# Performance work log

Measured on AMD Instinct MI355X. Metric: run time of the kernel, lower is better.

## Reference

```python
import jax, jax.numpy as jnp
import numpy as np


def _unfold3(x):
    # x: (B, 1, H, W) -> (B, 9, L), L=(H-2)*(W-2); kernel positions row-major (matches torch Unfold)
    B, _, H, W = x.shape
    patches = jnp.stack(
        [x[:, 0, i:H - 2 + i, j:W - 2 + j] for i in range(3) for j in range(3)], axis=1
    )  # (B, 9, H-2, W-2)
    return patches.reshape(B, 9, (H - 2) * (W - 2))


def setup_inputs() -> dict:
    key = jax.random.key(0)
    k1, k2, k3 = jax.random.split(key, 3)
    B, H, Wd = 16, 64, 64
    D = 32  # dendrite
    x = jax.random.uniform(k1, (B, 1, H, Wd), dtype=jnp.float32) * 255.0
    W = 0.01 * jnp.abs(jax.random.normal(k2, (D, 18, 4), dtype=jnp.float32)) + 0.2
    q = 0.01 * jnp.abs(jax.random.normal(k3, (D, 18, 4), dtype=jnp.float32)) + 0.0
    return {"x": x, "W": W, "q": q}


def reference(x, W, q):
    K_SYN = 10.0   # DConvSynaps k
    K_SOMA = 10.0  # DConvSoma slope
    p = _unfold3(x)                   # (B, 9, L)
    center = p[:, 4:5, :]             # (B, 1, L) center pixel of each 3x3 patch
    # torch.isclose(p, center, rtol=0, atol=3) -> |p - center| <= 3
    x1 = (jnp.abs(p - center) <= 3.0).astype(p.dtype)
    x1 = x1.at[:, 4, :].set(1.0)
    feat = jnp.concatenate([x1, p], axis=1)            # (B, 18, L)
    # DConvSynaps broadcast: (B, L, 1, 18, 1) against W,q (D, 18, 4)
    xb = feat.transpose(0, 2, 1)[:, :, None, :, None]  # (B, L, 1, 18, 1)
    syn = jax.nn.sigmoid((xb * W - q) * K_SYN)         # (B, L, D, 18, 4)
    dend = jnp.prod(syn, axis=3)                       # (B, L, D, 4)
    menb = jnp.sum(dend, axis=2)                       # (B, L, 4)
    soma = jax.nn.sigmoid((menb - 0.5) * K_SOMA)       # (B, L, 4)
    return jnp.sum(soma, axis=1)                       # (B, 4)
```

## Files before the change

kernel.cpp:

```cpp
#include <hip/hip_runtime.h>
#include <math.h>

#define LOG2E 1.44269504088896340736f

__global__ __launch_bounds__(256, 4)
void orientation_kernel(const float* __restrict__ x,
                        const float* __restrict__ Wm,
                        const float* __restrict__ qm,
                        float* __restrict__ out)
{
    const int blk  = blockIdx.x;
    const int b    = blk / 62;
    const int r    = blk - b * 62;
    const int tid  = threadIdx.x;
    const int wave = tid >> 6;
    const int lane = tid & 63;
    const int d    = lane & 31;
    const int kh   = lane >> 5;

    __shared__ float xs[3][64];
    __shared__ float red[4][4];

    if (tid < 192) {
        const int row = tid >> 6;
        const int col = tid & 63;
        xs[row][col] = x[b * 4096 + (r + row) * 64 + col];
    }
    __syncthreads();

    float s0v[2][9], dsv[2][9], Wc[2][9], qc[2][9];
#pragma unroll
    for (int kk = 0; kk < 2; ++kk) {
        const int k = kh + 2 * kk;
        const int base = d * 72;
#pragma unroll
        for (int j = 0; j < 9; ++j) {
            const float w0 = Wm[base + j * 4 + k];
            const float q0 = qm[base + j * 4 + k];
            const float e0 = __builtin_amdgcn_exp2f( 10.f * LOG2E * q0);
            const float s0 = __builtin_amdgcn_rcpf(1.f + e0);
            const float e1 = __builtin_amdgcn_exp2f(-10.f * LOG2E * (w0 - q0));
            const float s1 = __builtin_amdgcn_rcpf(1.f + e1);
            s0v[kk][j] = s0;
            dsv[kk][j] = s1 - s0;
            const float w1 = Wm[base + (9 + j) * 4 + k];
            const float q1 = qm[base + (9 + j) * 4 + k];
            Wc[kk][j] = -10.f * LOG2E * w1;
            qc[kk][j] =  10.f * LOG2E * q1;
        }
    }

    float acc0 = 0.f, acc1 = 0.f;

    const int c0 = wave * 16;
    const int c1 = (c0 + 16 < 62) ? (c0 + 16) : 62;

    for (int c = c0; c < c1; ++c) {
        float p[9];
#pragma unroll
        for (int i = 0; i < 3; ++i)
#pragma unroll
            for (int jj = 0; jj < 3; ++jj)
                p[i * 3 + jj] = xs[i][c + jj];
        const float ctr = p[4];

        float prodB0 = 1.f, prodB1 = 1.f;
        float prodA0 = 1.f, prodA1 = 1.f;
#pragma unroll
        for (int j = 0; j < 9; ++j) {
            const float x1f = (fabsf(p[j] - ctr) <= 3.0f) ? 1.f : 0.f;
            prodB0 *= fmaf(x1f, dsv[0][j], s0v[0][j]);
            prodB1 *= fmaf(x1f, dsv[1][j], s0v[1][j]);
            const float eA0 = __builtin_amdgcn_exp2f(fmaf(p[j], Wc[0][j], qc[0][j]));
            const float eA1 = __builtin_amdgcn_exp2f(fmaf(p[j], Wc[1][j], qc[1][j]));
            prodA0 = fmaf(prodA0, eA0, prodA0);
            prodA1 = fmaf(prodA1, eA1, prodA1);
        }
        float dend0 = prodB0 * __builtin_amdgcn_rcpf(prodA0);
        float dend1 = prodB1 * __builtin_amdgcn_rcpf(prodA1);

#pragma unroll
        for (int m = 1; m <= 16; m <<= 1) {
            dend0 += __shfl_xor(dend0, m, 64);
            dend1 += __shfl_xor(dend1, m, 64);
        }

        const float soma0 = __builtin_amdgcn_rcpf(
            1.f + __builtin_amdgcn_exp2f((0.5f - dend0) * (10.f * LOG2E)));
        const float soma1 = __builtin_amdgcn_rcpf(
            1.f + __builtin_amdgcn_exp2f((0.5f - dend1) * (10.f * LOG2E)));
        acc0 += soma0;
        acc1 += soma1;
    }

    if ((lane & 31) == 0) {
        red[wave][kh]     = acc0;
        red[wave][kh + 2] = acc1;
    }
    __syncthreads();

    if (tid < 4) {
        const float s = red[0][tid] + red[1][tid] + red[2][tid] + red[3][tid];
        atomicAdd(&out[b * 4 + tid], s);
    }
}

extern "C" void kernel_launch(void* const* d_in, const int* in_sizes, int n_in,
                              void* d_out, int out_size, void* d_ws, size_t ws_size,
                              hipStream_t stream) {
    const float* x  = (const float*)d_in[0];
    const float* Wm = (const float*)d_in[1];
    const float* qm = (const float*)d_in[2];
    float* out = (float*)d_out;

    const int B = in_sizes[0] / (64 * 64);

    hipMemsetAsync(d_out, 0, (size_t)out_size * sizeof(float), stream);

    dim3 grid(B * 62);
    dim3 block(256);
    orientation_kernel<<<grid, block, 0, stream>>>(x, Wm, qm, out);
}
```

Baseline: 52.65 us.

## Remap threads to pixel-per-lane with dendrite loop and shared param table

Switches the work decomposition from lanes over dendrites (with a shuffle reduction over 32 dendrites per pixel) to lanes over pixels, with each wave handling one output channel k and looping over all 32 dendrites serially. The per-(k,d,j) sigmoid constants are precomputed once per block into a 4608-entry float4 shared-memory table, and the center tap is special-cased. This removes the per-pixel cross-lane reductions and their soma work per chunk. In exchange, every block recomputes the full parameter table, which costs 4608 exp/rcp pairs plus global reads before any pixel work starts, and the inner loop now issues many LDS float4 loads.

```diff
diff --git a/kernel.cpp b/kernel.cpp
--- a/kernel.cpp
+++ b/kernel.cpp
@@ -2,6 +2,13 @@
 #include <math.h>
 
 #define LOG2E 1.44269504088896340736f
+
+constexpr int IMG  = 64;
+constexpr int OW   = 62;
+constexpr int NPIX = 62 * 62;
+constexpr int D    = 32;
+constexpr int K    = 4;
+constexpr int CHUNKS = (NPIX + 63) / 64;
 
 __global__ __launch_bounds__(256, 4)
 void orientation_kernel(const float* __restrict__ x,
@@ -9,100 +16,86 @@
                         const float* __restrict__ qm,
                         float* __restrict__ out)
 {
-    const int blk  = blockIdx.x;
-    const int b    = blk / 62;
-    const int r    = blk - b * 62;
-    const int tid  = threadIdx.x;
-    const int wave = tid >> 6;
-    const int lane = tid & 63;
-    const int d    = lane & 31;
-    const int kh   = lane >> 5;
+    __shared__ float4 tbl[K * D * 9];
 
-    __shared__ float xs[3][64];
-    __shared__ float red[4][4];
+    const int tid = threadIdx.x;
 
-    if (tid < 192) {
-        const int row = tid >> 6;
-        const int col = tid & 63;
-        xs[row][col] = x[b * 4096 + (r + row) * 64 + col];
+    for (int t = tid; t < K * D * 9; t += 256) {
+        const int j = t % 9;
+        const int dk = t / 9;
+        const int d = dk % D;
+        const int k = dk / D;
+        const int base = d * 72;
+
+        const float w0 = Wm[base + j * 4 + k];
+        const float q0 = qm[base + j * 4 + k];
+        const float s1 = __builtin_amdgcn_rcpf(
+            1.f + __builtin_amdgcn_exp2f(-10.f * LOG2E * (w0 - q0)));
+        float s0, ds;
+        if (j == 4) {
+            s0 = s1; ds = 0.f;
+        } else {
+            s0 = __builtin_amdgcn_rcpf(
+                1.f + __builtin_amdgcn_exp2f(10.f * LOG2E * q0));
+            ds = s1 - s0;
+        }
+        const float w1 = Wm[base + (9 + j) * 4 + k];
+        const float q1 = qm[base + (9 + j) * 4 + k];
+        tbl[t] = make_float4(s0, ds, -10.f * LOG2E * w1, 10.f * LOG2E * q1);
     }
     __syncthreads();
 
-    float s0v[2][9], dsv[2][9], Wc[2][9], qc[2][9];
+    const int lane = tid & 63;
+    const int k    = tid >> 6;
+    const int b     = blockIdx.x / CHUNKS;
+    const int chunk = blockIdx.x - b * CHUNKS;
+
+    const int pi    = chunk * 64 + lane;
+    const bool valid = (pi < NPIX);
+    const int pic   = valid ? pi : (NPIX - 1);
+    const int row   = pic / OW;
+    const int col   = pic - row * OW;
+
+    const float* xb = x + b * IMG * IMG;
+    float p[9];
 #pragma unroll
-    for (int kk = 0; kk < 2; ++kk) {
-        const int k = kh + 2 * kk;
-        const int base = d * 72;
+    for (int i = 0; i < 3; ++i)
+#pragma unroll
+        for (int jj = 0; jj < 3; ++jj)
+            p[i * 3 + jj] = xb[(row + i) * IMG + col + jj];
+
+    const float ctr = p[4];
+    float x1f[9];
+#pragma unroll
+    for (int j = 0; j < 9; ++j)
+        x1f[j] = (fabsf(p[j] - ctr) <= 3.0f) ? 1.f : 0.f;
+
+    const float4* tk = &tbl[k * D * 9];
+    float menb = 0.f;
+#pragma unroll 2
+    for (int d = 0; d < D; ++d) {
+        float prodB = 1.f;
+        float prodA = 1.f;
 #pragma unroll
         for (int j = 0; j < 9; ++j) {
-            const float w0 = Wm[base + j * 4 + k];
-            const float q0 = qm[base + j * 4 + k];
-            const float e0 = __builtin_amdgcn_exp2f( 10.f * LOG2E * q0);
-            const float s0 = __builtin_amdgcn_rcpf(1.f + e0);
-            const float e1 = __builtin_amdgcn_exp2f(-10.f * LOG2E * (w0 - q0));
-            const float s1 = __builtin_amdgcn_rcpf(1.f + e1);
-            s0v[kk][j] = s0;
-            dsv[kk][j] = s1 - s0;
-            const float w1 = Wm[base + (9 + j) * 4 + k];
-            const float q1 = qm[base + (9 + j) * 4 + k];
-            Wc[kk][j] = -10.f * LOG2E * w1;
-            qc[kk][j] =  10.f * LOG2E * q1;
+            const float4 c = tk[d * 9 + j];
+            prodB *= fmaf(x1f[j], c.y, c.x);
+            const float e = __builtin_amdgcn_exp2f(fmaf(p[j], c.z, c.w));
+            prodA = fmaf(prodA, e, prodA);
         }
+        menb += prodB * __builtin_amdgcn_rcpf(prodA);
     }
 
-    float acc0 = 0.f, acc1 = 0.f;
-
-    const int c0 = wave * 16;
-    const int c1 = (c0 + 16 < 62) ? (c0 + 16) : 62;
-
-    for (int c = c0; c < c1; ++c) {
-        float p[9];
-#pragma unroll
-        for (int i = 0; i < 3; ++i)
-#pragma unroll
-            for (int jj = 0; jj < 3; ++jj)
-                p[i * 3 + jj] = xs[i][c + jj];
-        const float ctr = p[4];
-
-        float prodB0 = 1.f, prodB1 = 1.f;
-        float prodA0 = 1.f, prodA1 = 1.f;
-#pragma unroll
-        for (int j = 0; j < 9; ++j) {
-            const float x1f = (fabsf(p[j] - ctr) <= 3.0f) ? 1.f : 0.f;
-            prodB0 *= fmaf(x1f, dsv[0][j], s0v[0][j]);
-            prodB1 *= fmaf(x1f, dsv[1][j], s0v[1][j]);
-            const float eA0 = __builtin_amdgcn_exp2f(fmaf(p[j], Wc[0][j], qc[0][j]));
-            const float eA1 = __builtin_amdgcn_exp2f(fmaf(p[j], Wc[1][j], qc[1][j]));
-            prodA0 = fmaf(prodA0, eA0, prodA0);
-            prodA1 = fmaf(prodA1, eA1, prodA1);
-        }
-        float dend0 = prodB0 * __builtin_amdgcn_rcpf(prodA0);
-        float dend1 = prodB1 * __builtin_amdgcn_rcpf(prodA1);
+    float soma = __builtin_amdgcn_rcpf(
+        1.f + __builtin_amdgcn_exp2f((0.5f - menb) * (10.f * LOG2E)));
+    if (!valid) soma = 0.f;
 
 #pragma unroll
-        for (int m = 1; m <= 16; m <<= 1) {
-            dend0 += __shfl_xor(dend0, m, 64);
-            dend1 += __shfl_xor(dend1, m, 64);
-        }
+    for (int m = 1; m <= 32; m <<= 1)
+        soma += __shfl_xor(soma, m, 64);
 
-        const float soma0 = __builtin_amdgcn_rcpf(
-            1.f + __builtin_amdgcn_exp2f((0.5f - dend0) * (10.f * LOG2E)));
-        const float soma1 = __builtin_amdgcn_rcpf(
-            1.f + __builtin_amdgcn_exp2f((0.5f - dend1) * (10.f * LOG2E)));
-        acc0 += soma0;
-        acc1 += soma1;
-    }
-
-    if ((lane & 31) == 0) {
-        red[wave][kh]     = acc0;
-        red[wave][kh + 2] = acc1;
-    }
-    __syncthreads();
-
-    if (tid < 4) {
-        const float s = red[0][tid] + red[1][tid] + red[2][tid] + red[3][tid];
-        atomicAdd(&out[b * 4 + tid], s);
-    }
+    if (lane == 0)
+        atomicAdd(&out[b * 4 + k], soma);
 }
 
 extern "C" void kernel_launch(void* const* d_in, const int* in_sizes, int n_in,
@@ -113,11 +106,11 @@
     const float* qm = (const float*)d_in[2];
     float* out = (float*)d_out;
 
-    const int B = in_sizes[0] / (64 * 64);
+    const int B = in_sizes[0] / (IMG * IMG);
 
     hipMemsetAsync(d_out, 0, (size_t)out_size * sizeof(float), stream);
 
-    dim3 grid(B * 62);
+    dim3 grid(B * CHUNKS);
     dim3 block(256);
     orientation_kernel<<<grid, block, 0, stream>>>(x, Wm, qm, out);
 }
```

New measurement: 45.35 us. 1.16x faster.

## Precompute synapse table in prologue kernel, use log-domain binary product and DPP reductions

Applied to the files above, without the earlier changes.

A small prologue kernel now precomputes per-(k,d) constants into workspace: the binary-feature sigmoid factors are turned into log2 terms, so their product becomes a sum of FMAs followed by one exp2. The same kernel zeroes the output, which replaces the memset. The main kernel loads this table with float4 reads instead of recomputing sigmoids in every block. The cross-lane reduction uses DPP adds for the first four steps, work is rebalanced across waves (16/16/15/15 pixels), and each wave issues atomics directly instead of doing a shared-memory block reduction. The tradeoffs are an extra kernel launch, more atomics and higher register use from the 64-entry tables.

```diff
diff --git a/kernel.cpp b/kernel.cpp
--- a/kernel.cpp
+++ b/kernel.cpp
@@ -3,105 +3,142 @@
 
 #define LOG2E 1.44269504088896340736f
 
+constexpr int IMG = 64;
+constexpr int OW  = 62;
+constexpr int D   = 32;
+constexpr int K   = 4;
+
+__global__ void build_table(const float* __restrict__ Wm,
+                            const float* __restrict__ qm,
+                            float* __restrict__ tb,
+                            float* __restrict__ out, int out_n)
+{
+    const int t = threadIdx.x;
+    for (int i = t; i < out_n; i += 128) out[i] = 0.f;
+    if (t >= K * D) return;
+    const int d = t & 31;
+    const int k = t >> 5;
+    const int base = d * 72;
+    float* e = tb + t * 32;
+
+    float cB = 0.f;
+    int jj = 0;
+#pragma unroll
+    for (int j = 0; j < 9; ++j) {
+        const float w0 = Wm[base + j * 4 + k];
+        const float q0 = qm[base + j * 4 + k];
+        const float l1 = -log2f(1.f + __builtin_amdgcn_exp2f(-10.f * LOG2E * (w0 - q0)));
+        if (j == 4) {
+            cB += l1;
+        } else {
+            const float l0 = -log2f(1.f + __builtin_amdgcn_exp2f(10.f * LOG2E * q0));
+            cB += l0;
+            e[jj++] = l1 - l0;
+        }
+        const float w1 = Wm[base + (9 + j) * 4 + k];
+        const float q1 = qm[base + (9 + j) * 4 + k];
+        e[9 + j]  = -10.f * LOG2E * w1;
+        e[18 + j] =  10.f * LOG2E * q1;
+    }
+    e[8] = cB;
+    e[27] = e[28] = e[29] = e[30] = e[31] = 0.f;
+}
+
+template <int CTRL>
+__device__ __forceinline__ float dpp_xadd(float v) {
+    const int t = __builtin_amdgcn_update_dpp(0, __float_as_int(v), CTRL, 0xf, 0xf, true);
+    return v + __int_as_float(t);
+}
+
 __global__ __launch_bounds__(256, 4)
-void orientation_kernel(const float* __restrict__ x,
-                        const float* __restrict__ Wm,
-                        const float* __restrict__ qm,
-                        float* __restrict__ out)
+void orientation_main(const float* __restrict__ x,
+                      const float4* __restrict__ tb,
+                      float* __restrict__ out)
 {
-    const int blk  = blockIdx.x;
-    const int b    = blk / 62;
-    const int r    = blk - b * 62;
     const int tid  = threadIdx.x;
     const int wave = tid >> 6;
     const int lane = tid & 63;
     const int d    = lane & 31;
     const int kh   = lane >> 5;
+    const int b    = blockIdx.x / OW;
+    const int r    = blockIdx.x - b * OW;
 
-    __shared__ float xs[3][64];
-    __shared__ float red[4][4];
-
+    __shared__ float xs[3][IMG];
     if (tid < 192) {
         const int row = tid >> 6;
         const int col = tid & 63;
-        xs[row][col] = x[b * 4096 + (r + row) * 64 + col];
+        xs[row][col] = x[b * IMG * IMG + (r + row) * IMG + col];
+    }
+
+    float E0[32], E1[32];
+    {
+        const float4* t0 = tb + (kh * D + d) * 8;
+        const float4* t1 = t0 + 2 * D * 8;
+#pragma unroll
+        for (int i = 0; i < 8; ++i) {
+            *reinterpret_cast<float4*>(&E0[4 * i]) = t0[i];
+            *reinterpret_cast<float4*>(&E1[4 * i]) = t1[i];
+        }
     }
     __syncthreads();
 
-    float s0v[2][9], dsv[2][9], Wc[2][9], qc[2][9];
+    const int npx = (wave < 2) ? 16 : 15;
+    const int c0  = wave * 16 - ((wave == 3) ? 1 : 0);
+
+    float acc0 = 0.f, acc1 = 0.f;
+    for (int ci = 0; ci < npx; ++ci) {
+        const int c = c0 + ci;
+        float p[9];
 #pragma unroll
-    for (int kk = 0; kk < 2; ++kk) {
-        const int k = kh + 2 * kk;
-        const int base = d * 72;
+        for (int i = 0; i < 3; ++i) {
+            p[i * 3 + 0] = xs[i][c + 0];
+            p[i * 3 + 1] = xs[i][c + 1];
+            p[i * 3 + 2] = xs[i][c + 2];
+        }
+        const float ctr = p[4];
+        float x1f[9];
+#pragma unroll
+        for (int j = 0; j < 9; ++j)
+            x1f[j] = (fabsf(p[j] - ctr) <= 3.0f) ? 1.f : 0.f;
+
+        float logB0 = E0[8], logB1 = E1[8];
+        {
+            int jj = 0;
+#pragma unroll
+            for (int j = 0; j < 9; ++j) {
+                if (j == 4) continue;
+                logB0 = fmaf(x1f[j], E0[jj], logB0);
+                logB1 = fmaf(x1f[j], E1[jj], logB1);
+                ++jj;
+            }
+        }
+        float pA0 = 1.f, pA1 = 1.f;
 #pragma unroll
         for (int j = 0; j < 9; ++j) {
-            const float w0 = Wm[base + j * 4 + k];
-            const float q0 = qm[base + j * 4 + k];
-            const float e0 = __builtin_amdgcn_exp2f( 10.f * LOG2E * q0);
-            const float s0 = __builtin_amdgcn_rcpf(1.f + e0);
-            const float e1 = __builtin_amdgcn_exp2f(-10.f * LOG2E * (w0 - q0));
-            const float s1 = __builtin_amdgcn_rcpf(1.f + e1);
-            s0v[kk][j] = s0;
-            dsv[kk][j] = s1 - s0;
-            const float w1 = Wm[base + (9 + j) * 4 + k];
-            const float q1 = qm[base + (9 + j) * 4 + k];
-            Wc[kk][j] = -10.f * LOG2E * w1;
-            qc[kk][j] =  10.f * LOG2E * q1;
+            const float a0 = fmaf(p[j], E0[9 + j], E0[18 + j]);
+            const float a1 = fmaf(p[j], E1[9 + j], E1[18 + j]);
+            pA0 = fmaf(pA0, __builtin_amdgcn_exp2f(a0), pA0);
+            pA1 = fmaf(pA1, __builtin_amdgcn_exp2f(a1), pA1);
         }
-    }
+        float v0 = __builtin_amdgcn_exp2f(logB0) * __builtin_amdgcn_rcpf(pA0);
+        float v1 = __builtin_amdgcn_exp2f(logB1) * __builtin_amdgcn_rcpf(pA1);
 
-    float acc0 = 0.f, acc1 = 0.f;
+        v0 = dpp_xadd<0xB1>(v0);   v1 = dpp_xadd<0xB1>(v1);
+        v0 = dpp_xadd<0x4E>(v0);   v1 = dpp_xadd<0x4E>(v1);
+        v0 = dpp_xadd<0x141>(v0);  v1 = dpp_xadd<0x141>(v1);
+        v0 = dpp_xadd<0x140>(v0);  v1 = dpp_xadd<0x140>(v1);
+        v0 += __shfl_xor(v0, 16, 64);
+        v1 += __shfl_xor(v1, 16, 64);
 
-    const int c0 = wave * 16;
-    const int c1 = (c0 + 16 < 62) ? (c0 + 16) : 62;
-
-    for (int c = c0; c < c1; ++c) {
-        float p[9];
-#pragma unroll
-        for (int i = 0; i < 3; ++i)
-#pragma unroll
-            for (int jj = 0; jj < 3; ++jj)
-                p[i * 3 + jj] = xs[i][c + jj];
-        const float ctr = p[4];
-
-        float prodB0 = 1.f, prodB1 = 1.f;
-        float prodA0 = 1.f, prodA1 = 1.f;
-#pragma unroll
-        for (int j = 0; j < 9; ++j) {
-            const float x1f = (fabsf(p[j] - ctr) <= 3.0f) ? 1.f : 0.f;
-            prodB0 *= fmaf(x1f, dsv[0][j], s0v[0][j]);
-            prodB1 *= fmaf(x1f, dsv[1][j], s0v[1][j]);
-            const float eA0 = __builtin_amdgcn_exp2f(fmaf(p[j], Wc[0][j], qc[0][j]));
-            const float eA1 = __builtin_amdgcn_exp2f(fmaf(p[j], Wc[1][j], qc[1][j]));
-            prodA0 = fmaf(prodA0, eA0, prodA0);
-            prodA1 = fmaf(prodA1, eA1, prodA1);
-        }
-        float dend0 = prodB0 * __builtin_amdgcn_rcpf(prodA0);
-        float dend1 = prodB1 * __builtin_amdgcn_rcpf(prodA1);
-
-#pragma unroll
-        for (int m = 1; m <= 16; m <<= 1) {
-            dend0 += __shfl_xor(dend0, m, 64);
-            dend1 += __shfl_xor(dend1, m, 64);
-        }
-
-        const float soma0 = __builtin_amdgcn_rcpf(
-            1.f + __builtin_amdgcn_exp2f((0.5f - dend0) * (10.f * LOG2E)));
-        const float soma1 = __builtin_amdgcn_rcpf(
-            1.f + __builtin_amdgcn_exp2f((0.5f - dend1) * (10.f * LOG2E)));
-        acc0 += soma0;
-        acc1 += soma1;
+        acc0 += __builtin_amdgcn_rcpf(
+            1.f + __builtin_amdgcn_exp2f(fmaf(v0, -10.f * LOG2E, 5.f * LOG2E)));
+        acc1 += __builtin_amdgcn_rcpf(
+            1.f + __builtin_amdgcn_exp2f(fmaf(v1, -10.f * LOG2E, 5.f * LOG2E)));
     }
 
     if ((lane & 31) == 0) {
-        red[wave][kh]     = acc0;
-        red[wave][kh + 2] = acc1;
-    }
-    __syncthreads();
-
-    if (tid < 4) {
-        const float s = red[0][tid] + red[1][tid] + red[2][tid] + red[3][tid];
-        atomicAdd(&out[b * 4 + tid], s);
+        atomicAdd(&out[b * 4 + kh],     acc0);
+        atomicAdd(&out[b * 4 + kh + 2], acc1);
     }
 }
 
@@ -112,12 +149,13 @@
     const float* Wm = (const float*)d_in[1];
     const float* qm = (const float*)d_in[2];
     float* out = (float*)d_out;
+    float* tb  = (float*)d_ws;
 
-    const int B = in_sizes[0] / (64 * 64);
+    const int B = in_sizes[0] / (IMG * IMG);
 
-    hipMemsetAsync(d_out, 0, (size_t)out_size * sizeof(float), stream);
+    build_table<<<1, 128, 0, stream>>>(Wm, qm, tb, out, out_size);
 
-    dim3 grid(B * 62);
+    dim3 grid(B * OW);
     dim3 block(256);
-    orientation_kernel<<<grid, block, 0, stream>>>(x, Wm, qm, out);
+    orientation_main<<<grid, block, 0, stream>>>(x, (const float4*)tb, out);
 }
```

Result: slower. 77.19 us (+46.6%).
